# Performance work log

Measured on AMD Instinct MI355X. Metric: run time of the kernel, lower is better.

The kernel has to match this reference:

```python
import jax, jax.numpy as jnp
import numpy as np

N = 100000
E = 1600000
F_IN = 128
HID = 64
C_OUT = 40


def gcn_conv(x, src, dst, W, b):
    # PyG GCNConv: linear transform, then symmetric-normalized sum aggregation
    n = x.shape[0]
    x = x @ W  # [N, out]
    deg = jax.ops.segment_sum(jnp.ones_like(src, dtype=x.dtype), dst, num_segments=n)
    dinv = jnp.where(deg > 0, jax.lax.rsqrt(deg), 0.0).astype(x.dtype)
    norm = dinv[src] * dinv[dst]  # [E']
    msgs = x[src] * norm[:, None]  # gather + scale
    out = jax.ops.segment_sum(msgs, dst, num_segments=n)  # scatter-add
    return out + b


def setup_inputs() -> dict:
    key = jax.random.key(0)
    k1, k2, k3, k4, k5, k6 = jax.random.split(key, 6)
    x = jax.random.normal(k1, (N, F_IN), dtype=jnp.float32)
    edge_index = jax.random.randint(k2, (2, E), 0, N, dtype=jnp.int64)
    # Glorot-style init for GCNConv linear weights, zero bias (PyG default)
    W1 = jax.random.normal(k3, (F_IN, HID), dtype=jnp.float32) / np.sqrt(F_IN)
    b1 = jnp.zeros((HID,), dtype=jnp.float32)
    W2 = jax.random.normal(k4, (HID, C_OUT), dtype=jnp.float32) / np.sqrt(HID)
    b2 = jnp.zeros((C_OUT,), dtype=jnp.float32)
    return {"x": x, "edge_index": edge_index, "W1": W1, "b1": b1, "W2": W2, "b2": b2}


def reference(x, edge_index, W1, b1, W2, b2):
    n = x.shape[0]
    # add self-loops (PyG GCNConv default add_self_loops=True)
    loops = jnp.arange(n, dtype=edge_index.dtype)
    src = jnp.concatenate([edge_index[0], loops])
    dst = jnp.concatenate([edge_index[1], loops])
    h = gcn_conv(x, src, dst, W1, b1)
    h = jax.nn.relu(h)
    # F.dropout with training=False is identity (eval-mode reference)
    out = gcn_conv(h, src, dst, W2, b2)
    return out
```

## Files before the change

kernel.cpp:

```cpp
#include <hip/hip_runtime.h>

#define F_IN 128
#define HID 64
#define C_OUT 40

#define RB_SHIFT 6
#define RB 64
#define CAP 1408
#define NBMAX 2048
#define FILL_CHUNK 4096
#define FILL_THREADS 512

typedef unsigned short ushort_t;
typedef unsigned int uint_t;
typedef __attribute__((ext_vector_type(8))) short bf16x8;
typedef __attribute__((ext_vector_type(4))) float f32x4;

__device__ __forceinline__ ushort_t f2bf(float f) {
    uint_t u = __float_as_uint(f);
    return (ushort_t)((u + 0x7FFF + ((u >> 16) & 1)) >> 16);
}
__device__ __forceinline__ uint_t cvtpk(float lo, float hi) {
    uint_t r;
    asm("v_cvt_pk_bf16_f32 %0, %1, %2" : "=v"(r) : "v"(lo), "v"(hi));
    return r;
}
__device__ __forceinline__ float bf_lo(uint_t u) { return __uint_as_float(u << 16); }
__device__ __forceinline__ float bf_hi(uint_t u) { return __uint_as_float(u & 0xFFFF0000u); }
__device__ __forceinline__ bf16x8 u4_to_bf(uint4 u) {
    union { uint4 a; bf16x8 b; } cv; cv.a = u; return cv.b;
}

#define ACC8(u) { a[0] += bf_lo(u.x); a[1] += bf_hi(u.x); a[2] += bf_lo(u.y); a[3] += bf_hi(u.y); \
                  a[4] += bf_lo(u.z); a[5] += bf_hi(u.z); a[6] += bf_lo(u.w); a[7] += bf_hi(u.w); }

__global__ __launch_bounds__(FILL_THREADS) void bucket_fill_kernel(
    const int* __restrict__ src, const int* __restrict__ dst, int E,
    int* __restrict__ gtail, int* __restrict__ buckets, int NB)
{
    __shared__ int lcnt[NBMAX];
    __shared__ int lbase[NBMAX];
    int t = threadIdx.x;
    for (int i = t; i < NBMAX; i += FILL_THREADS) lcnt[i] = 0;
    __syncthreads();
    int base = blockIdx.x * FILL_CHUNK;
    #pragma unroll
    for (int k = 0; k < FILL_CHUNK / FILL_THREADS; ++k) {
        int e = base + k * FILL_THREADS + t;
        if (e < E) atomicAdd(&lcnt[dst[e] >> RB_SHIFT], 1);
    }
    __syncthreads();
    for (int b = t; b < NB; b += FILL_THREADS) {
        int c = lcnt[b];
        if (c > 0) lbase[b] = b * CAP + atomicAdd(&gtail[b], c);
    }
    __syncthreads();
    #pragma unroll
    for (int k = 0; k < FILL_CHUNK / FILL_THREADS; ++k) {
        int e = base + k * FILL_THREADS + t;
        if (e < E) {
            int d = dst[e], s = src[e];
            int b = d >> RB_SHIFT;
            int pos = atomicAdd(&lbase[b], 1);
            if (pos < (b + 1) * CAP) buckets[pos] = (s << RB_SHIFT) | (d & (RB - 1));
        }
    }
}

__global__ __launch_bounds__(256) void csr_sort_kernel(
    const int* __restrict__ gtail, const int* __restrict__ buckets,
    int* __restrict__ csr, int* __restrict__ begp, int* __restrict__ degp,
    float* __restrict__ dinv, int N)
{
    __shared__ int hist[RB];
    __shared__ int cursor[RB];
    int t = threadIdx.x;
    int b = blockIdx.x;
    if (t < RB) hist[t] = 0;
    __syncthreads();
    int cnt = gtail[b];
    int base = b * CAP;
    for (int i = t; i < cnt; i += 256) atomicAdd(&hist[buckets[base + i] & (RB - 1)], 1);
    __syncthreads();
    if (t < RB) {
        int v = hist[t];
        int incl = v;
        #pragma unroll
        for (int off = 1; off < 64; off <<= 1) {
            int u = __shfl_up(incl, off);
            if (t >= off) incl += u;
        }
        int excl = incl - v;
        cursor[t] = excl;
        int node = b * RB + t;
        if (node < N) {
            begp[node] = base + excl;
            degp[node] = v;
            dinv[node] = rsqrtf((float)(v + 1));
        }
    }
    __syncthreads();
    for (int i = t; i < cnt; i += 256) {
        int e = buckets[base + i];
        int n = e & (RB - 1);
        int r = atomicAdd(&cursor[n], 1);
        csr[base + r] = e >> RB_SHIFT;
    }
}

__global__ void wconv_kernel(const float* __restrict__ W1, const float* __restrict__ W2,
                             ushort_t* __restrict__ wb1, ushort_t* __restrict__ wb2,
                             int* __restrict__ gtail, int NB)
{
    int tid = blockIdx.x * 256 + threadIdx.x;
    if (tid < NB) gtail[tid] = 0;
    if (tid < 8192) {
        int j = tid & 7, l = (tid >> 3) & 63, ks = (tid >> 9) & 3, ct = tid >> 11;
        int c = ct * 16 + (l & 15);
        int k = ks * 32 + (l >> 4) * 8 + j;
        wb1[tid] = f2bf(W1[k * HID + c]);
    } else if (tid < 8192 + 3072) {
        int s = tid - 8192;
        int j = s & 7, l = (s >> 3) & 63, ks = (s >> 9) & 1, ct = s >> 10;
        int c = ct * 16 + (l & 15);
        int k = ks * 32 + (l >> 4) * 8 + j;
        wb2[s] = (c < C_OUT) ? f2bf(W2[k * C_OUT + c]) : (ushort_t)0;
    }
}

__global__ __launch_bounds__(256) void gemm1_mfma(
    const float* __restrict__ x, const uint_t* __restrict__ Wb,
    const float* __restrict__ dinv, uint_t* __restrict__ y, int N)
{
    __shared__ uint_t ldsW[4096];
    int t = threadIdx.x;
    {
        const uint4* s4 = (const uint4*)Wb;
        uint4* d4 = (uint4*)ldsW;
        for (int i = t; i < 1024; i += 256) d4[i] = s4[i];
    }
    __syncthreads();
    int wid = t >> 6, lane = t & 63;
    int m = lane & 15, kb = lane >> 4;
    int wr = blockIdx.x * 128 + wid * 32;
    int ra0 = min(wr + m, N - 1);
    int ra1 = min(wr + 16 + m, N - 1);
    f32x4 acc[2][4] = {};
    #pragma unroll
    for (int ks = 0; ks < 4; ++ks) {
        const float* p0 = &x[(size_t)ra0 * F_IN + ks * 32 + kb * 8];
        const float* p1 = &x[(size_t)ra1 * F_IN + ks * 32 + kb * 8];
        float4 a0 = *(const float4*)p0, a1 = *(const float4*)(p0 + 4);
        float4 c0 = *(const float4*)p1, c1 = *(const float4*)(p1 + 4);
        uint4 ua = make_uint4(cvtpk(a0.x, a0.y), cvtpk(a0.z, a0.w),
                              cvtpk(a1.x, a1.y), cvtpk(a1.z, a1.w));
        uint4 ub = make_uint4(cvtpk(c0.x, c0.y), cvtpk(c0.z, c0.w),
                              cvtpk(c1.x, c1.y), cvtpk(c1.z, c1.w));
        bf16x8 fa0 = u4_to_bf(ua), fa1 = u4_to_bf(ub);
        #pragma unroll
        for (int ct = 0; ct < 4; ++ct) {
            uint4 wu = *(uint4*)&ldsW[((ct * 4 + ks) * 64 + lane) * 4];
            bf16x8 fb = u4_to_bf(wu);
            acc[0][ct] = __builtin_amdgcn_mfma_f32_16x16x32_bf16(fa0, fb, acc[0][ct], 0, 0, 0);
            acc[1][ct] = __builtin_amdgcn_mfma_f32_16x16x32_bf16(fa1, fb, acc[1][ct], 0, 0, 0);
        }
    }
    int rq = lane >> 4;
    #pragma unroll
    for (int rt = 0; rt < 2; ++rt) {
        float dv[4]; int rows[4];
        #pragma unroll
        for (int j = 0; j < 4; ++j) {
            int r = wr + rt * 16 + rq * 4 + j;
            rows[j] = r;
            dv[j] = dinv[min(r, N - 1)];
        }
        #pragma unroll
        for (int ct = 0; ct < 4; ++ct) {
            #pragma unroll
            for (int j = 0; j < 4; ++j) {
                float v = acc[rt][ct][j] * dv[j];
                float pv = __shfl_xor(v, 1);
                if (!(lane & 1) && rows[j] < N) {
                    y[(size_t)rows[j] * 32 + ct * 8 + (m >> 1)] = cvtpk(v, pv);
                }
            }
        }
    }
}

__global__ __launch_bounds__(256) void agg1_kernel(
    const int* __restrict__ csr, const int* __restrict__ begp, const int* __restrict__ degp,
    const uint_t* __restrict__ y, const float* __restrict__ dinv,
    const float* __restrict__ bias, uint_t* __restrict__ h, int N)
{
    int node = blockIdx.x * 4 + (threadIdx.x >> 6);
    if (node >= N) return;
    int lane = threadIdx.x & 63;
    int o = lane >> 3;
    int c = lane & 7;
    int beg = begp[node];
    int end = beg + degp[node];
    float a[8] = {};
    if (o == 0) {
        uint4 u = *(const uint4*)&y[node * 32 + c * 4];
        ACC8(u);
    }
    int j = beg;
    for (; j + 15 < end; j += 16) {
        int e0 = csr[j + o];
        int e1 = csr[j + 8 + o];
        uint4 u0 = *(const uint4*)&y[e0 * 32 + c * 4];
        uint4 u1 = *(const uint4*)&y[e1 * 32 + c * 4];
        ACC8(u0);
        ACC8(u1);
    }
    for (; j < end; j += 8) {
        if (j + o < end) {
            int e = csr[j + o];
            uint4 u = *(const uint4*)&y[e * 32 + c * 4];
            ACC8(u);
        }
    }
    #pragma unroll
    for (int k = 0; k < 8; ++k) {
        a[k] += __shfl_xor(a[k], 8);
        a[k] += __shfl_xor(a[k], 16);
        a[k] += __shfl_xor(a[k], 32);
    }
    if (o == 0) {
        float di = dinv[node];
        float4 b0 = *(const float4*)&bias[c * 8];
        float4 b1 = *(const float4*)&bias[c * 8 + 4];
        float o0 = fmaxf(a[0] * di + b0.x, 0.f);
        float o1 = fmaxf(a[1] * di + b0.y, 0.f);
        float o2 = fmaxf(a[2] * di + b0.z, 0.f);
        float o3 = fmaxf(a[3] * di + b0.w, 0.f);
        float o4 = fmaxf(a[4] * di + b1.x, 0.f);
        float o5 = fmaxf(a[5] * di + b1.y, 0.f);
        float o6 = fmaxf(a[6] * di + b1.z, 0.f);
        float o7 = fmaxf(a[7] * di + b1.w, 0.f);
        uint4 r = make_uint4(cvtpk(o0, o1), cvtpk(o2, o3), cvtpk(o4, o5), cvtpk(o6, o7));
        *(uint4*)&h[node * 32 + c * 4] = r;
    }
}

__global__ __launch_bounds__(256) void gemm2_mfma(
    const uint_t* __restrict__ h, const uint_t* __restrict__ Wb,
    const float* __restrict__ dinv, uint_t* __restrict__ y, int N)
{
    __shared__ uint_t ldsW[1536];
    int t = threadIdx.x;
    {
        const uint4* s4 = (const uint4*)Wb;
        uint4* d4 = (uint4*)ldsW;
        for (int i = t; i < 384; i += 256) d4[i] = s4[i];
    }
    __syncthreads();
    int wid = t >> 6, lane = t & 63;
    int m = lane & 15, kb = lane >> 4;
    int wr = blockIdx.x * 128 + wid * 32;
    int ra0 = min(wr + m, N - 1);
    int ra1 = min(wr + 16 + m, N - 1);
    f32x4 acc[2][3] = {};
    #pragma unroll
    for (int ks = 0; ks < 2; ++ks) {
        uint4 ua = *(const uint4*)&h[(size_t)ra0 * 32 + ks * 16 + kb * 4];
        uint4 ub = *(const uint4*)&h[(size_t)ra1 * 32 + ks * 16 + kb * 4];
        bf16x8 fa0 = u4_to_bf(ua), fa1 = u4_to_bf(ub);
        #pragma unroll
        for (int ct = 0; ct < 3; ++ct) {
            uint4 wu = *(uint4*)&ldsW[((ct * 2 + ks) * 64 + lane) * 4];
            bf16x8 fb = u4_to_bf(wu);
            acc[0][ct] = __builtin_amdgcn_mfma_f32_16x16x32_bf16(fa0, fb, acc[0][ct], 0, 0, 0);
            acc[1][ct] = __builtin_amdgcn_mfma_f32_16x16x32_bf16(fa1, fb, acc[1][ct], 0, 0, 0);
        }
    }
    int rq = lane >> 4;
    #pragma unroll
    for (int rt = 0; rt < 2; ++rt) {
        float dv[4]; int rows[4];
        #pragma unroll
        for (int j = 0; j < 4; ++j) {
            int r = wr + rt * 16 + rq * 4 + j;
            rows[j] = r;
            dv[j] = dinv[min(r, N - 1)];
        }
        #pragma unroll
        for (int ct = 0; ct < 3; ++ct) {
            #pragma unroll
            for (int j = 0; j < 4; ++j) {
                float v = acc[rt][ct][j] * dv[j];
                float pv = __shfl_xor(v, 1);
                bool colok = (ct < 2) || (m < 8);
                if (!(lane & 1) && colok && rows[j] < N) {
                    y[(size_t)rows[j] * 32 + ct * 8 + (m >> 1)] = cvtpk(v, pv);
                }
            }
        }
    }
}

__global__ __launch_bounds__(256) void agg2_kernel(
    const int* __restrict__ csr, const int* __restrict__ begp, const int* __restrict__ degp,
    const uint_t* __restrict__ y, const float* __restrict__ dinv,
    const float* __restrict__ bias, float* __restrict__ out, int N)
{
    int node = blockIdx.x * 4 + (threadIdx.x >> 6);
    if (node >= N) return;
    int lane = threadIdx.x & 63;
    int o = lane >> 3;
    int c = lane & 7;
    bool act = (c < 5);
    int beg = begp[node];
    int end = beg + degp[node];
    float a[8] = {};
    if (o == 0 && act) {
        uint4 u = *(const uint4*)&y[node * 32 + c * 4];
        ACC8(u);
    }
    int j = beg;
    for (; j + 15 < end; j += 16) {
        if (act) {
            int e0 = csr[j + o];
            int e1 = csr[j + 8 + o];
            uint4 u0 = *(const uint4*)&y[e0 * 32 + c * 4];
            uint4 u1 = *(const uint4*)&y[e1 * 32 + c * 4];
            ACC8(u0);
            ACC8(u1);
        }
    }
    for (; j < end; j += 8) {
        if (j + o < end && act) {
            int e = csr[j + o];
            uint4 u = *(const uint4*)&y[e * 32 + c * 4];
            ACC8(u);
        }
    }
    #pragma unroll
    for (int k = 0; k < 8; ++k) {
        a[k] += __shfl_xor(a[k], 8);
        a[k] += __shfl_xor(a[k], 16);
        a[k] += __shfl_xor(a[k], 32);
    }
    if (o == 0 && act) {
        float di = dinv[node];
        float4 b0 = *(const float4*)&bias[c * 8];
        float4 b1 = *(const float4*)&bias[c * 8 + 4];
        float4 r0, r1;
        r0.x = a[0] * di + b0.x;
        r0.y = a[1] * di + b0.y;
        r0.z = a[2] * di + b0.z;
        r0.w = a[3] * di + b0.w;
        r1.x = a[4] * di + b1.x;
        r1.y = a[5] * di + b1.y;
        r1.z = a[6] * di + b1.z;
        r1.w = a[7] * di + b1.w;
        *(float4*)&out[(size_t)node * C_OUT + c * 8] = r0;
        *(float4*)&out[(size_t)node * C_OUT + c * 8 + 4] = r1;
    }
}

extern "C" void kernel_launch(void* const* d_in, const int* in_sizes, int n_in,
                              void* d_out, int out_size, void* d_ws, size_t ws_size,
                              hipStream_t stream)
{
    const float* x  = (const float*)d_in[0];
    const int*   ei = (const int*)d_in[1];
    const float* W1 = (const float*)d_in[2];
    const float* b1 = (const float*)d_in[3];
    const float* W2 = (const float*)d_in[4];
    const float* b2 = (const float*)d_in[5];
    float* out = (float*)d_out;

    int N = in_sizes[0] / F_IN;
    int E = in_sizes[1] / 2;
    const int* src = ei;
    const int* dst = ei + E;
    int NB = (N + RB - 1) / RB;
    int NBLK = (N + 127) / 128;

    char* ws = (char*)d_ws;
    uint_t* y1b    = (uint_t*)ws;  ws += (size_t)N * 32 * 4;
    uint_t* y2b    = (uint_t*)ws;  ws += (size_t)N * 32 * 4;
    uint_t* h1p    = (uint_t*)ws;  ws += (size_t)N * 32 * 4;
    float* dinv    = (float*)ws;   ws += (size_t)N * 4;
    int*   begp    = (int*)ws;     ws += (size_t)N * 4;
    int*   degp    = (int*)ws;     ws += (size_t)N * 4;
    int*   gtail   = (int*)ws;     ws += (size_t)NB * 4;
    int*   buckets = (int*)ws;     ws += (size_t)NB * CAP * 4;
    int*   csr     = (int*)ws;     ws += (size_t)NB * CAP * 4;
    ushort_t* wb1  = (ushort_t*)ws; ws += 8192 * 2;
    ushort_t* wb2  = (ushort_t*)ws; ws += 3072 * 2;

    wconv_kernel<<<44, 256, 0, stream>>>(W1, W2, wb1, wb2, gtail, NB);

    bucket_fill_kernel<<<(E + FILL_CHUNK - 1) / FILL_CHUNK, FILL_THREADS, 0, stream>>>(
        src, dst, E, gtail, buckets, NB);
    csr_sort_kernel<<<NB, 256, 0, stream>>>(gtail, buckets, csr, begp, degp, dinv, N);

    gemm1_mfma<<<NBLK, 256, 0, stream>>>(x, (const uint_t*)wb1, dinv, y1b, N);
    agg1_kernel<<<(N + 3) / 4, 256, 0, stream>>>(csr, begp, degp, y1b, dinv, b1, h1p, N);

    gemm2_mfma<<<NBLK, 256, 0, stream>>>(h1p, (const uint_t*)wb2, dinv, y2b, N);
    agg2_kernel<<<(N + 3) / 4, 256, 0, stream>>>(csr, begp, degp, y2b, dinv, b2, out, N);
}
```

Before: 156.6 us.

## Replace global-atomic bucket fill with per-chunk local sort and gather

```diff
diff --git a/kernel.cpp b/kernel.cpp
--- a/kernel.cpp
+++ b/kernel.cpp
@@ -8,7 +8,7 @@
 #define RB 64
 #define CAP 1408
 #define NBMAX 2048
-#define FILL_CHUNK 4096
+#define FILL_CHUNK 8192
 #define FILL_THREADS 512
 
 typedef unsigned short ushort_t;
@@ -34,86 +34,152 @@
 #define ACC8(u) { a[0] += bf_lo(u.x); a[1] += bf_hi(u.x); a[2] += bf_lo(u.y); a[3] += bf_hi(u.y); \
                   a[4] += bf_lo(u.z); a[5] += bf_hi(u.z); a[6] += bf_lo(u.w); a[7] += bf_hi(u.w); }
 
-__global__ __launch_bounds__(FILL_THREADS) void bucket_fill_kernel(
+__global__ __launch_bounds__(FILL_THREADS) void bsort_kernel(
     const int* __restrict__ src, const int* __restrict__ dst, int E,
-    int* __restrict__ gtail, int* __restrict__ buckets, int NB)
+    int* __restrict__ hist, int* __restrict__ bm, int NB)
 {
     __shared__ int lcnt[NBMAX];
-    __shared__ int lbase[NBMAX];
+    __shared__ int loff[NBMAX];
+    __shared__ int wsum[8];
     int t = threadIdx.x;
     for (int i = t; i < NBMAX; i += FILL_THREADS) lcnt[i] = 0;
     __syncthreads();
     int base = blockIdx.x * FILL_CHUNK;
+    int nE = min(E - base, FILL_CHUNK);
     #pragma unroll
     for (int k = 0; k < FILL_CHUNK / FILL_THREADS; ++k) {
-        int e = base + k * FILL_THREADS + t;
-        if (e < E) atomicAdd(&lcnt[dst[e] >> RB_SHIFT], 1);
-    }
-    __syncthreads();
-    for (int b = t; b < NB; b += FILL_THREADS) {
-        int c = lcnt[b];
-        if (c > 0) lbase[b] = b * CAP + atomicAdd(&gtail[b], c);
-    }
+        int e = k * FILL_THREADS + t;
+        if (e < nE) atomicAdd(&lcnt[dst[base + e] >> RB_SHIFT], 1);
+    }
+    __syncthreads();
+    {
+        int v[4]; int tsum = 0;
+        #pragma unroll
+        for (int i = 0; i < 4; ++i) { v[i] = lcnt[t * 4 + i]; tsum += v[i]; }
+        int lane = t & 63, wid = t >> 6;
+        int incl = tsum;
+        #pragma unroll
+        for (int off = 1; off < 64; off <<= 1) {
+            int u = __shfl_up(incl, off);
+            if (lane >= off) incl += u;
+        }
+        if (lane == 63) wsum[wid] = incl;
+        __syncthreads();
+        if (t < 8) {
+            int w = wsum[t];
+            int wincl = w;
+            #pragma unroll
+            for (int off = 1; off < 8; off <<= 1) {
+                int u = __shfl_up(wincl, off);
+                if (t >= off) wincl += u;
+            }
+            wsum[t] = wincl - w;
+        }
+        __syncthreads();
+        int run = wsum[wid] + incl - tsum;
+        #pragma unroll
+        for (int i = 0; i < 4; ++i) { loff[t * 4 + i] = run; run += v[i]; }
+    }
+    __syncthreads();
+    long long hrow = (long long)blockIdx.x * (NB + 1);
+    for (int i = t; i < NB; i += FILL_THREADS) hist[hrow + i] = loff[i];
+    if (t == 0) hist[hrow + NB] = nE;
     __syncthreads();
     #pragma unroll
     for (int k = 0; k < FILL_CHUNK / FILL_THREADS; ++k) {
-        int e = base + k * FILL_THREADS + t;
-        if (e < E) {
-            int d = dst[e], s = src[e];
+        int e = k * FILL_THREADS + t;
+        if (e < nE) {
+            int d = dst[base + e], s = src[base + e];
             int b = d >> RB_SHIFT;
-            int pos = atomicAdd(&lbase[b], 1);
-            if (pos < (b + 1) * CAP) buckets[pos] = (s << RB_SHIFT) | (d & (RB - 1));
-        }
-    }
-}
-
-__global__ __launch_bounds__(256) void csr_sort_kernel(
-    const int* __restrict__ gtail, const int* __restrict__ buckets,
+            int pos = atomicAdd(&loff[b], 1);
+            bm[base + pos] = (s << RB_SHIFT) | (d & (RB - 1));
+        }
+    }
+}
+
+__global__ __launch_bounds__(256) void csr_gather_kernel(
+    const int* __restrict__ hist, const int* __restrict__ bm, int K,
     int* __restrict__ csr, int* __restrict__ begp, int* __restrict__ degp,
-    float* __restrict__ dinv, int N)
-{
-    __shared__ int hist[RB];
+    float* __restrict__ dinv, int N, int NB)
+{
+    __shared__ int staging[CAP];
+    __shared__ int histo[RB];
     __shared__ int cursor[RB];
+    __shared__ int waux[8];
     int t = threadIdx.x;
     int b = blockIdx.x;
-    if (t < RB) hist[t] = 0;
-    __syncthreads();
-    int cnt = gtail[b];
-    int base = b * CAP;
-    for (int i = t; i < cnt; i += 256) atomicAdd(&hist[buckets[base + i] & (RB - 1)], 1);
+    int len = 0, st = 0;
+    if (t < K) {
+        long long hrow = (long long)t * (NB + 1);
+        st = hist[hrow + b];
+        len = hist[hrow + b + 1] - st;
+    }
+    int lane = t & 63, wid = t >> 6;
+    int incl = len;
+    #pragma unroll
+    for (int off = 1; off < 64; off <<= 1) {
+        int u = __shfl_up(incl, off);
+        if (lane >= off) incl += u;
+    }
+    if (lane == 63) waux[wid] = incl;
+    if (t < RB) histo[t] = 0;
+    __syncthreads();
+    if (t < 4) {
+        int w = waux[t];
+        int wincl = w;
+        #pragma unroll
+        for (int off = 1; off < 4; off <<= 1) {
+            int u = __shfl_up(wincl, off);
+            if (t >= off) wincl += u;
+        }
+        waux[t] = wincl - w;
+        if (t == 3) waux[4] = wincl;
+    }
+    __syncthreads();
+    int bpos = waux[wid] + incl - len;
+    int cnt = waux[4];
+    if (cnt > CAP) cnt = CAP;
+    if (t < K && len > 0) {
+        int gbase = t * FILL_CHUNK + st;
+        for (int i = 0; i < len; ++i) {
+            int p = bpos + i;
+            if (p < CAP) staging[p] = bm[gbase + i];
+        }
+    }
+    __syncthreads();
+    for (int i = t; i < cnt; i += 256) atomicAdd(&histo[staging[i] & (RB - 1)], 1);
     __syncthreads();
     if (t < RB) {
-        int v = hist[t];
-        int incl = v;
+        int v = histo[t];
+        int nincl = v;
         #pragma unroll
         for (int off = 1; off < 64; off <<= 1) {
-            int u = __shfl_up(incl, off);
-            if (t >= off) incl += u;
-        }
-        int excl = incl - v;
+            int u = __shfl_up(nincl, off);
+            if (t >= off) nincl += u;
+        }
+        int excl = nincl - v;
         cursor[t] = excl;
         int node = b * RB + t;
         if (node < N) {
-            begp[node] = base + excl;
+            begp[node] = b * CAP + excl;
             degp[node] = v;
             dinv[node] = rsqrtf((float)(v + 1));
         }
     }
     __syncthreads();
+    int cbase = b * CAP;
     for (int i = t; i < cnt; i += 256) {
-        int e = buckets[base + i];
+        int e = staging[i];
         int n = e & (RB - 1);
         int r = atomicAdd(&cursor[n], 1);
-        csr[base + r] = e >> RB_SHIFT;
+        csr[cbase + r] = e >> RB_SHIFT;
     }
 }
 
 __global__ void wconv_kernel(const float* __restrict__ W1, const float* __restrict__ W2,
-                             ushort_t* __restrict__ wb1, ushort_t* __restrict__ wb2,
-                             int* __restrict__ gtail, int NB)
+                             ushort_t* __restrict__ wb1, ushort_t* __restrict__ wb2)
 {
     int tid = blockIdx.x * 256 + threadIdx.x;
-    if (tid < NB) gtail[tid] = 0;
     if (tid < 8192) {
         int j = tid & 7, l = (tid >> 3) & 63, ks = (tid >> 9) & 3, ct = tid >> 11;
         int c = ct * 16 + (l & 15);
@@ -378,6 +444,7 @@
     const int* src = ei;
     const int* dst = ei + E;
     int NB = (N + RB - 1) / RB;
+    int K = (E + FILL_CHUNK - 1) / FILL_CHUNK;
     int NBLK = (N + 127) / 128;
 
     char* ws = (char*)d_ws;
@@ -387,17 +454,16 @@
     float* dinv    = (float*)ws;   ws += (size_t)N * 4;
     int*   begp    = (int*)ws;     ws += (size_t)N * 4;
     int*   degp    = (int*)ws;     ws += (size_t)N * 4;
-    int*   gtail   = (int*)ws;     ws += (size_t)NB * 4;
-    int*   buckets = (int*)ws;     ws += (size_t)NB * CAP * 4;
+    int*   hist    = (int*)ws;     ws += (size_t)K * (NB + 1) * 4;
+    int*   bm      = (int*)ws;     ws += (size_t)K * FILL_CHUNK * 4;
     int*   csr     = (int*)ws;     ws += (size_t)NB * CAP * 4;
     ushort_t* wb1  = (ushort_t*)ws; ws += 8192 * 2;
     ushort_t* wb2  = (ushort_t*)ws; ws += 3072 * 2;
 
-    wconv_kernel<<<44, 256, 0, stream>>>(W1, W2, wb1, wb2, gtail, NB);
-
-    bucket_fill_kernel<<<(E + FILL_CHUNK - 1) / FILL_CHUNK, FILL_THREADS, 0, stream>>>(
-        src, dst, E, gtail, buckets, NB);
-    csr_sort_kernel<<<NB, 256, 0, stream>>>(gtail, buckets, csr, begp, degp, dinv, N);
+    wconv_kernel<<<44, 256, 0, stream>>>(W1, W2, wb1, wb2);
+
+    bsort_kernel<<<K, FILL_THREADS, 0, stream>>>(src, dst, E, hist, bm, NB);
+    csr_gather_kernel<<<NB, 256, 0, stream>>>(hist, bm, K, csr, begp, degp, dinv, N, NB);
 
     gemm1_mfma<<<NBLK, 256, 0, stream>>>(x, (const uint_t*)wb1, dinv, y1b, N);
     agg1_kernel<<<(N + 3) / 4, 256, 0, stream>>>(csr, begp, degp, y1b, dinv, b1, h1p, N);
```

After: 154.6 us. Within noise of the previous version (-1.3%).
